# Kernel tuning notes

Measured on AMD Instinct MI355X. Metric: run time of the kernel, lower is better.

The kernel has to match this reference:

```python
import jax, jax.numpy as jnp
import numpy as np

H, D = 16, 64  # num_attention_heads, attention_head_size
BASE = 10000.0

def _rope(q, k, seq_len):
    # RotaryPositionalEmbedding: inv_freq over arange(0, D, 2); emb = cat(freqs, freqs)
    inv_freq = 1.0 / (BASE ** (jnp.arange(0, D, 2, dtype=jnp.float32) / D))  # [D/2]=32
    pos = jnp.arange(seq_len, dtype=jnp.float32)
    freqs = jnp.outer(pos, inv_freq)            # [S, 32]; equals cos_emb[..., :d]
    cos, sin = jnp.cos(freqs), jnp.sin(freqs)   # [S, 32]
    d = D // 2                                   # 32: only first half of head dim rotated
    half = d // 2                                # 16: internal rotate-half within rot part
    def rot(x):  # x: [B, H, S, D]
        xr, xp = x[..., :d], x[..., d:]
        swapped = jnp.concatenate([xr[..., half:], xr[..., :half]], axis=-1)
        xr2 = xr * cos - swapped * sin
        return jnp.concatenate([xr2, xp], axis=-1)
    return rot(q), rot(k)

def setup_inputs() -> dict:
    key = jax.random.key(0)
    ks = jax.random.split(key, 9)
    B, S, E = 2, 2048, 1024
    std = 0.02  # initializer_range
    inp = {"hidden_states": jax.random.normal(ks[0], (B, S, E), jnp.float32)}
    for i, n in enumerate(["q", "k", "v", "d"]):
        inp[f"W{n}"] = jax.random.normal(ks[1 + 2 * i], (E, E), jnp.float32) * std
        inp[f"b{n}"] = jnp.zeros((E,), jnp.float32)
    return inp

def reference(hidden_states, Wq, bq, Wk, bk, Wv, bv, Wd, bd):
    B, S, E = hidden_states.shape
    def heads(x):  # [B,S,E] -> [B,H,S,D]
        return x.reshape(B, S, H, D).transpose(0, 2, 1, 3)
    q = heads(hidden_states @ Wq + bq)
    k = heads(hidden_states @ Wk + bk)
    v = heads(hidden_states @ Wv + bv)
    q, k = _rope(q, k, S)
    scores = jnp.einsum("bhqd,bhkd->bhqk", q, k) / jnp.sqrt(jnp.float32(D))
    causal = jnp.tril(jnp.ones((S, S), dtype=bool))
    scores = jnp.where(causal, scores, -jnp.inf)
    probs = jax.nn.softmax(scores, axis=-1)
    ctx = jnp.einsum("bhqk,bhkd->bhqd", probs, v)
    ctx = ctx.transpose(0, 2, 1, 3).reshape(B, S, E)
    return ctx @ Wd + bd
```

## Files before the change

kernel.cpp:

```cpp
#include <hip/hip_runtime.h>
#include <stdint.h>

typedef __bf16 bf8 __attribute__((ext_vector_type(8)));
typedef float f4 __attribute__((ext_vector_type(4)));
typedef unsigned short us8 __attribute__((ext_vector_type(8)));
typedef unsigned short us4 __attribute__((ext_vector_type(4)));

#define MFMA16(a, b, c) __builtin_amdgcn_mfma_f32_16x16x32_bf16(a, b, c, 0, 0, 0)

__device__ __forceinline__ unsigned short f2b(float f) {
  union { float f; unsigned u; } x; x.f = f;
  unsigned u = x.u;
  u += 0x7fffu + ((u >> 16) & 1u);
  return (unsigned short)(u >> 16);
}

__device__ __forceinline__ unsigned pk2(float a, float b) {
  union { float f; unsigned u; } ua, ub; ua.f = a; ub.f = b;
  return __builtin_amdgcn_perm(ub.u + 0x8000u, ua.u + 0x8000u, 0x07060302u);
}

__global__ __launch_bounds__(256) void cvt_bf16_kernel(
    const float* __restrict__ x, unsigned short* __restrict__ y) {
  int i = blockIdx.x * 256 + threadIdx.x;
  float4 v = ((const float4*)x)[i];
  us4 r = { f2b(v.x), f2b(v.y), f2b(v.z), f2b(v.w) };
  *(us4*)(y + (size_t)i * 4) = r;
}

__global__ __launch_bounds__(256) void transpose_cvt_kernel(
    const float* __restrict__ W, unsigned short* __restrict__ Wt) {
  __shared__ float tile[32][33];
  int tx = threadIdx.x & 31, ty = threadIdx.x >> 5;
  int kb = blockIdx.x * 32, nb = blockIdx.y * 32;
#pragma unroll
  for (int j = 0; j < 32; j += 8)
    tile[ty + j][tx] = W[(size_t)(kb + ty + j) * 1024 + nb + tx];
  __syncthreads();
#pragma unroll
  for (int j = 0; j < 32; j += 8)
    Wt[(size_t)(nb + ty + j) * 1024 + kb + tx] = f2b(tile[tx][ty + j]);
}

#define LDSK 40

__global__ __launch_bounds__(256) void gemm_qkv_kernel(
    const unsigned short* __restrict__ X,
    const unsigned short* __restrict__ Wqt, const unsigned short* __restrict__ Wkt,
    const unsigned short* __restrict__ Wvt,
    const float* __restrict__ bq, const float* __restrict__ bk,
    const float* __restrict__ bv,
    unsigned short* __restrict__ Qo, unsigned short* __restrict__ Ko,
    unsigned short* __restrict__ Vo) {
  const unsigned short* Wt; const float* bias; unsigned short* out;
  if (blockIdx.z == 0)      { Wt = Wqt; bias = bq; out = Qo; }
  else if (blockIdx.z == 1) { Wt = Wkt; bias = bk; out = Ko; }
  else                      { Wt = Wvt; bias = bv; out = Vo; }

  __shared__ unsigned short As[128 * LDSK];
  __shared__ unsigned short Bs[128 * LDSK];
  const int t = threadIdx.x;
  const int wave = t >> 6, lane = t & 63, quad = lane >> 4, l16 = lane & 15;
  const int wm = (wave >> 1) * 64, wn = (wave & 1) * 64;
  const int m0 = blockIdx.y * 128, n0 = blockIdx.x * 128;

  f4 acc[4][4];
#pragma unroll
  for (int mi = 0; mi < 4; ++mi)
#pragma unroll
    for (int ni = 0; ni < 4; ++ni) acc[mi][ni] = (f4)0.0f;

  for (int k0 = 0; k0 < 1024; k0 += 32) {
    __syncthreads();
#pragma unroll
    for (int it = 0; it < 2; ++it) {
      int chunk = t + it * 256;
      int row = chunk >> 2, c8 = (chunk & 3) * 8;
      *(us8*)&As[row * LDSK + c8] =
          *(const us8*)&X[(size_t)(m0 + row) * 1024 + k0 + c8];
      *(us8*)&Bs[row * LDSK + c8] =
          *(const us8*)&Wt[(size_t)(n0 + row) * 1024 + k0 + c8];
    }
    __syncthreads();
    bf8 a[4], b[4];
#pragma unroll
    for (int mi = 0; mi < 4; ++mi)
      a[mi] = *(const bf8*)&As[(wm + mi * 16 + l16) * LDSK + quad * 8];
#pragma unroll
    for (int ni = 0; ni < 4; ++ni)
      b[ni] = *(const bf8*)&Bs[(wn + ni * 16 + l16) * LDSK + quad * 8];
#pragma unroll
    for (int mi = 0; mi < 4; ++mi)
#pragma unroll
      for (int ni = 0; ni < 4; ++ni)
        acc[mi][ni] = MFMA16(a[mi], b[ni], acc[mi][ni]);
  }

  float biasv[4];
#pragma unroll
  for (int ni = 0; ni < 4; ++ni) biasv[ni] = bias[n0 + wn + ni * 16 + l16];

  if (blockIdx.z < 2) {
    const float kr = 13.287712379549449f / 32.0f;
    const float f0 = exp2f(-(float)l16 * kr);
    const float f1 = exp2f(-(float)(l16 + 16) * kr);
    const float qs = (blockIdx.z == 0) ? 0.18033688011112042f : 1.0f;
#pragma unroll
    for (int mi = 0; mi < 4; ++mi) {
#pragma unroll
      for (int r = 0; r < 4; ++r) {
        int m = m0 + wm + mi * 16 + quad * 4 + r;
        float s = (float)(m & 2047);
        float s0, c0, s1, c1;
        __sincosf(s * f0, &s0, &c0);
        __sincosf(s * f1, &s1, &c1);
        float v0 = acc[mi][0][r] + biasv[0];
        float v1 = acc[mi][1][r] + biasv[1];
        acc[mi][0][r] = (v0 * c0 - v1 * s0) * qs;
        acc[mi][1][r] = (v1 * c1 - v0 * s1) * qs;
        acc[mi][2][r] = (acc[mi][2][r] + biasv[2]) * qs;
        acc[mi][3][r] = (acc[mi][3][r] + biasv[3]) * qs;
      }
    }
#pragma unroll
    for (int ni = 0; ni < 4; ++ni) {
      int n = n0 + wn + ni * 16 + l16;
      int h = n >> 6, d = n & 63;
#pragma unroll
      for (int mi = 0; mi < 4; ++mi) {
#pragma unroll
        for (int r = 0; r < 4; ++r) {
          int m = m0 + wm + mi * 16 + quad * 4 + r;
          int b_ = m >> 11, s = m & 2047;
          out[(size_t)(((b_ << 4) | h) * 2048 + s) * 64 + d] = f2b(acc[mi][ni][r]);
        }
      }
    }
  } else {
#pragma unroll
    for (int ni = 0; ni < 4; ++ni) {
      int n = n0 + wn + ni * 16 + l16;
      int h = n >> 6, d = n & 63;
#pragma unroll
      for (int mi = 0; mi < 4; ++mi) {
        int m = m0 + wm + mi * 16 + quad * 4;
        int b_ = m >> 11, s = m & 2047;
        us4 w = { f2b(acc[mi][ni][0] + biasv[ni]), f2b(acc[mi][ni][1] + biasv[ni]),
                  f2b(acc[mi][ni][2] + biasv[ni]), f2b(acc[mi][ni][3] + biasv[ni]) };
        *(us4*)&out[((size_t)(((b_ << 4) | h) * 64 + d)) * 2048 + s] = w;
      }
    }
  }
}

__global__ __launch_bounds__(256) void flash_attn_kernel(
    const unsigned short* __restrict__ Q, const unsigned short* __restrict__ K,
    const unsigned short* __restrict__ Vt, unsigned short* __restrict__ ctx) {
  __shared__ unsigned short PsT[4][16 * 72];

  const int t = threadIdx.x;
  const int wave = t >> 6, lane = t & 63, quad = lane >> 4, l16 = lane & 15;

  const int id = blockIdx.x;
  const int bh = id & 31;
  const int j = id >> 5;
  const int qt = (j >> 3) ? (15 - (j & 7)) : (j & 7);
  const int qbase = qt * 128;
  const int b = bh >> 4, h = bh & 15;

  const unsigned short* Qh = Q + (size_t)bh * 2048 * 64;
  const unsigned short* Kh = K + (size_t)bh * 2048 * 64;
  const unsigned short* Vh = Vt + (size_t)bh * 64 * 2048;

  const int wrow0 = qbase + wave * 32;

  bf8 qb[2][2];
#pragma unroll
  for (int f = 0; f < 2; ++f)
#pragma unroll
    for (int c = 0; c < 2; ++c)
      qb[f][c] = *(const bf8*)&Qh[(size_t)(wrow0 + f * 16 + l16) * 64 + c * 32 + quad * 8];

  us8 ones_u = { 0x3F80, 0x3F80, 0x3F80, 0x3F80, 0x3F80, 0x3F80, 0x3F80, 0x3F80 };
  bf8 ones = *(bf8*)&ones_u;

  f4 o[2][4];
  float mrow[2] = { -3e38f, -3e38f }, lrow[2] = { 0.0f, 0.0f };
#pragma unroll
  for (int f = 0; f < 2; ++f)
#pragma unroll
    for (int dt = 0; dt < 4; ++dt) o[f][dt] = (f4)0.0f;

  unsigned short* myP = &PsT[wave][0];
  const int nkw = (wrow0 >> 6) + 1;

  for (int kt = 0; kt < nkw; ++kt) {
    const int k0 = kt * 64;
    bf8 ka[4][2], va[4][2];
#pragma unroll
    for (int mt = 0; mt < 4; ++mt)
#pragma unroll
      for (int c = 0; c < 2; ++c)
        ka[mt][c] = *(const bf8*)&Kh[(size_t)(k0 + mt * 16 + l16) * 64 + c * 32 + quad * 8];
#pragma unroll
    for (int dt = 0; dt < 4; ++dt)
#pragma unroll
      for (int c = 0; c < 2; ++c)
        va[dt][c] = *(const bf8*)&Vh[(size_t)(dt * 16 + l16) * 2048 + k0 + c * 32 + quad * 8];

#pragma unroll
    for (int f = 0; f < 2; ++f) {
      const int q = wrow0 + f * 16 + l16;
      f4 sc[4];
#pragma unroll
      for (int mt = 0; mt < 4; ++mt) {
        f4 z = (f4)0.0f;
        z = MFMA16(ka[mt][0], qb[f][0], z);
        z = MFMA16(ka[mt][1], qb[f][1], z);
        sc[mt] = z;
      }
      if (k0 + 63 > wrow0 + f * 16) {
#pragma unroll
        for (int mt = 0; mt < 4; ++mt)
#pragma unroll
          for (int r = 0; r < 4; ++r) {
            int kk = k0 + mt * 16 + quad * 4 + r;
            if (kk > q) sc[mt][r] = -3e38f;
          }
      }
      float mx = fmaxf(fmaxf(sc[0][0], sc[0][1]), fmaxf(sc[0][2], sc[0][3]));
#pragma unroll
      for (int mt = 1; mt < 4; ++mt)
        mx = fmaxf(mx, fmaxf(fmaxf(sc[mt][0], sc[mt][1]), fmaxf(sc[mt][2], sc[mt][3])));
      mx = fmaxf(mx, __shfl_xor(mx, 16));
      mx = fmaxf(mx, __shfl_xor(mx, 32));
      float mn = fmaxf(mrow[f], mx);
      float al = exp2f(mrow[f] - mn);
      mrow[f] = mn;
#pragma unroll
      for (int mt = 0; mt < 4; ++mt) {
        float p0 = exp2f(sc[mt][0] - mn), p1 = exp2f(sc[mt][1] - mn);
        float p2 = exp2f(sc[mt][2] - mn), p3 = exp2f(sc[mt][3] - mn);
        uint2 w = { pk2(p0, p1), pk2(p2, p3) };
        *(uint2*)&myP[l16 * 72 + mt * 16 + quad * 4] = w;
      }
#pragma unroll
      for (int dt = 0; dt < 4; ++dt) o[f][dt] *= al;
      __threadfence_block();
      bf8 pb0 = *(const bf8*)&myP[l16 * 72 + quad * 8];
      bf8 pb1 = *(const bf8*)&myP[l16 * 72 + 32 + quad * 8];
      f4 z2 = (f4)0.0f;
      z2 = MFMA16(ones, pb0, z2);
      z2 = MFMA16(ones, pb1, z2);
      lrow[f] = lrow[f] * al + z2[0];
#pragma unroll
      for (int dt = 0; dt < 4; ++dt) {
        o[f][dt] = MFMA16(va[dt][0], pb0, o[f][dt]);
        o[f][dt] = MFMA16(va[dt][1], pb1, o[f][dt]);
      }
    }
  }

#pragma unroll
  for (int f = 0; f < 2; ++f) {
    float inv = 1.0f / lrow[f];
    int q = wrow0 + f * 16 + l16;
#pragma unroll
    for (int dt = 0; dt < 4; ++dt) {
      us4 w = { f2b(o[f][dt][0] * inv), f2b(o[f][dt][1] * inv),
                f2b(o[f][dt][2] * inv), f2b(o[f][dt][3] * inv) };
      *(us4*)&ctx[((size_t)(b * 2048 + q)) * 1024 + h * 64 + dt * 16 + quad * 4] = w;
    }
  }
}

__global__ __launch_bounds__(256) void gemm_out_kernel(
    const unsigned short* __restrict__ A,
    const unsigned short* __restrict__ Wt,
    const float* __restrict__ bias, float* __restrict__ out) {
  __shared__ unsigned short As[128 * LDSK];
  __shared__ unsigned short Bs[128 * LDSK];
  const int t = threadIdx.x;
  const int wave = t >> 6, lane = t & 63, quad = lane >> 4, l16 = lane & 15;
  const int wm = (wave >> 1) * 64, wn = (wave & 1) * 64;
  const int m0 = blockIdx.y * 128, n0 = blockIdx.x * 128;

  f4 acc[4][4];
#pragma unroll
  for (int mi = 0; mi < 4; ++mi)
#pragma unroll
    for (int ni = 0; ni < 4; ++ni) acc[mi][ni] = (f4)0.0f;

  for (int k0 = 0; k0 < 1024; k0 += 32) {
    __syncthreads();
#pragma unroll
    for (int it = 0; it < 2; ++it) {
      int chunk = t + it * 256;
      int row = chunk >> 2, c8 = (chunk & 3) * 8;
      *(us8*)&As[row * LDSK + c8] =
          *(const us8*)&A[(size_t)(m0 + row) * 1024 + k0 + c8];
      *(us8*)&Bs[row * LDSK + c8] =
          *(const us8*)&Wt[(size_t)(n0 + row) * 1024 + k0 + c8];
    }
    __syncthreads();
    bf8 a[4], b[4];
#pragma unroll
    for (int mi = 0; mi < 4; ++mi)
      a[mi] = *(const bf8*)&As[(wm + mi * 16 + l16) * LDSK + quad * 8];
#pragma unroll
    for (int ni = 0; ni < 4; ++ni)
      b[ni] = *(const bf8*)&Bs[(wn + ni * 16 + l16) * LDSK + quad * 8];
#pragma unroll
    for (int mi = 0; mi < 4; ++mi)
#pragma unroll
      for (int ni = 0; ni < 4; ++ni)
        acc[mi][ni] = MFMA16(a[mi], b[ni], acc[mi][ni]);
  }
#pragma unroll
  for (int ni = 0; ni < 4; ++ni) {
    int n = n0 + wn + ni * 16 + l16;
    float bv_ = bias[n];
#pragma unroll
    for (int mi = 0; mi < 4; ++mi) {
#pragma unroll
      for (int r = 0; r < 4; ++r) {
        int m = m0 + wm + mi * 16 + quad * 4 + r;
        out[(size_t)m * 1024 + n] = acc[mi][ni][r] + bv_;
      }
    }
  }
}

extern "C" void kernel_launch(void* const* d_in, const int* in_sizes, int n_in,
                              void* d_out, int out_size, void* d_ws, size_t ws_size,
                              hipStream_t stream) {
  const float* hidden = (const float*)d_in[0];
  const float* Wq = (const float*)d_in[1];
  const float* bq = (const float*)d_in[2];
  const float* Wk = (const float*)d_in[3];
  const float* bk = (const float*)d_in[4];
  const float* Wv = (const float*)d_in[5];
  const float* bv = (const float*)d_in[6];
  const float* Wd = (const float*)d_in[7];
  const float* bd = (const float*)d_in[8];
  float* out = (float*)d_out;

  char* ws = (char*)d_ws;
  unsigned short* Xb  = (unsigned short*)(ws);
  unsigned short* Wqt = (unsigned short*)(ws + ( 8ull << 20));
  unsigned short* Wkt = (unsigned short*)(ws + (10ull << 20));
  unsigned short* Wvt = (unsigned short*)(ws + (12ull << 20));
  unsigned short* Wdt = (unsigned short*)(ws + (14ull << 20));
  unsigned short* Qb  = (unsigned short*)(ws + (16ull << 20));
  unsigned short* Kb  = (unsigned short*)(ws + (24ull << 20));
  unsigned short* Vb  = (unsigned short*)(ws + (32ull << 20));
  unsigned short* Cb  = (unsigned short*)(ws + (40ull << 20));

  cvt_bf16_kernel<<<4096, 256, 0, stream>>>(hidden, Xb);
  dim3 tg(32, 32);
  transpose_cvt_kernel<<<tg, 256, 0, stream>>>(Wq, Wqt);
  transpose_cvt_kernel<<<tg, 256, 0, stream>>>(Wk, Wkt);
  transpose_cvt_kernel<<<tg, 256, 0, stream>>>(Wv, Wvt);
  transpose_cvt_kernel<<<tg, 256, 0, stream>>>(Wd, Wdt);
  gemm_qkv_kernel<<<dim3(8, 32, 3), 256, 0, stream>>>(
      Xb, Wqt, Wkt, Wvt, bq, bk, bv, Qb, Kb, Vb);
  flash_attn_kernel<<<512, 256, 0, stream>>>(Qb, Kb, Vb, Cb);
  gemm_out_kernel<<<dim3(8, 32), 256, 0, stream>>>(Cb, Wdt, bd, out);
}
```

Baseline: 240.9 us.

## Switch flash attention to 32x32 MFMA with K/V double-buffering and merge weight transposes

Rewrites the attention inner loop to use 32x32x16 bf16 MFMA tiles, so each wave handles 32 query rows as one fragment. K/V loads for the next 64-key tile are prefetched into a second register set while the current tile computes. The row sum is now accumulated in VALU with a cross-half shuffle instead of an extra MFMA against a ones vector, and the LDS fence becomes an explicit lgkmcnt wait. The four weight transpose launches are merged into one launch with a z-dimension. Double-buffered fragments raise register pressure, which the occupancy hint of 2 blocks per CU may constrain.

```diff
diff --git a/kernel.cpp b/kernel.cpp
--- a/kernel.cpp
+++ b/kernel.cpp
@@ -3,10 +3,12 @@
 
 typedef __bf16 bf8 __attribute__((ext_vector_type(8)));
 typedef float f4 __attribute__((ext_vector_type(4)));
+typedef float f16v __attribute__((ext_vector_type(16)));
 typedef unsigned short us8 __attribute__((ext_vector_type(8)));
 typedef unsigned short us4 __attribute__((ext_vector_type(4)));
 
 #define MFMA16(a, b, c) __builtin_amdgcn_mfma_f32_16x16x32_bf16(a, b, c, 0, 0, 0)
+#define MFMA32(a, b, c) __builtin_amdgcn_mfma_f32_32x32x16_bf16(a, b, c, 0, 0, 0)
 
 __device__ __forceinline__ unsigned short f2b(float f) {
   union { float f; unsigned u; } x; x.f = f;
@@ -28,8 +30,16 @@
   *(us4*)(y + (size_t)i * 4) = r;
 }
 
-__global__ __launch_bounds__(256) void transpose_cvt_kernel(
-    const float* __restrict__ W, unsigned short* __restrict__ Wt) {
+__global__ __launch_bounds__(256) void transpose_cvt4_kernel(
+    const float* __restrict__ W0, const float* __restrict__ W1,
+    const float* __restrict__ W2, const float* __restrict__ W3,
+    unsigned short* __restrict__ T0, unsigned short* __restrict__ T1,
+    unsigned short* __restrict__ T2, unsigned short* __restrict__ T3) {
+  const float* W; unsigned short* Wt;
+  if (blockIdx.z == 0)      { W = W0; Wt = T0; }
+  else if (blockIdx.z == 1) { W = W1; Wt = T1; }
+  else if (blockIdx.z == 2) { W = W2; Wt = T2; }
+  else                      { W = W3; Wt = T3; }
   __shared__ float tile[32][33];
   int tx = threadIdx.x & 31, ty = threadIdx.x >> 5;
   int kb = blockIdx.x * 32, nb = blockIdx.y * 32;
@@ -153,13 +163,16 @@
   }
 }
 
-__global__ __launch_bounds__(256) void flash_attn_kernel(
+#define PST 72
+
+__global__ __launch_bounds__(256, 2) void flash_attn_kernel(
     const unsigned short* __restrict__ Q, const unsigned short* __restrict__ K,
     const unsigned short* __restrict__ Vt, unsigned short* __restrict__ ctx) {
-  __shared__ unsigned short PsT[4][16 * 72];
+  __shared__ unsigned short PsT[4][32 * PST];
 
   const int t = threadIdx.x;
-  const int wave = t >> 6, lane = t & 63, quad = lane >> 4, l16 = lane & 15;
+  const int wave = t >> 6, lane = t & 63;
+  const int l32 = lane & 31, hl = lane >> 5;
 
   const int id = blockIdx.x;
   const int bh = id & 31;
@@ -173,104 +186,111 @@
   const unsigned short* Vh = Vt + (size_t)bh * 64 * 2048;
 
   const int wrow0 = qbase + wave * 32;
-
-  bf8 qb[2][2];
-#pragma unroll
-  for (int f = 0; f < 2; ++f)
-#pragma unroll
-    for (int c = 0; c < 2; ++c)
-      qb[f][c] = *(const bf8*)&Qh[(size_t)(wrow0 + f * 16 + l16) * 64 + c * 32 + quad * 8];
-
-  us8 ones_u = { 0x3F80, 0x3F80, 0x3F80, 0x3F80, 0x3F80, 0x3F80, 0x3F80, 0x3F80 };
-  bf8 ones = *(bf8*)&ones_u;
-
-  f4 o[2][4];
-  float mrow[2] = { -3e38f, -3e38f }, lrow[2] = { 0.0f, 0.0f };
-#pragma unroll
-  for (int f = 0; f < 2; ++f)
-#pragma unroll
-    for (int dt = 0; dt < 4; ++dt) o[f][dt] = (f4)0.0f;
+  const int q = wrow0 + l32;
+
+  bf8 qb[4];
+#pragma unroll
+  for (int c = 0; c < 4; ++c)
+    qb[c] = *(const bf8*)&Qh[(size_t)q * 64 + c * 16 + hl * 8];
+
+  f16v o0 = (f16v)0.0f, o1 = (f16v)0.0f;
+  float mrow = -3e38f, lrow = 0.0f;
 
   unsigned short* myP = &PsT[wave][0];
   const int nkw = (wrow0 >> 6) + 1;
 
-  for (int kt = 0; kt < nkw; ++kt) {
-    const int k0 = kt * 64;
-    bf8 ka[4][2], va[4][2];
-#pragma unroll
-    for (int mt = 0; mt < 4; ++mt)
-#pragma unroll
-      for (int c = 0; c < 2; ++c)
-        ka[mt][c] = *(const bf8*)&Kh[(size_t)(k0 + mt * 16 + l16) * 64 + c * 32 + quad * 8];
-#pragma unroll
-    for (int dt = 0; dt < 4; ++dt)
-#pragma unroll
-      for (int c = 0; c < 2; ++c)
-        va[dt][c] = *(const bf8*)&Vh[(size_t)(dt * 16 + l16) * 2048 + k0 + c * 32 + quad * 8];
-
-#pragma unroll
-    for (int f = 0; f < 2; ++f) {
-      const int q = wrow0 + f * 16 + l16;
-      f4 sc[4];
-#pragma unroll
-      for (int mt = 0; mt < 4; ++mt) {
-        f4 z = (f4)0.0f;
-        z = MFMA16(ka[mt][0], qb[f][0], z);
-        z = MFMA16(ka[mt][1], qb[f][1], z);
-        sc[mt] = z;
-      }
-      if (k0 + 63 > wrow0 + f * 16) {
-#pragma unroll
-        for (int mt = 0; mt < 4; ++mt)
-#pragma unroll
-          for (int r = 0; r < 4; ++r) {
-            int kk = k0 + mt * 16 + quad * 4 + r;
-            if (kk > q) sc[mt][r] = -3e38f;
-          }
-      }
-      float mx = fmaxf(fmaxf(sc[0][0], sc[0][1]), fmaxf(sc[0][2], sc[0][3]));
-#pragma unroll
-      for (int mt = 1; mt < 4; ++mt)
-        mx = fmaxf(mx, fmaxf(fmaxf(sc[mt][0], sc[mt][1]), fmaxf(sc[mt][2], sc[mt][3])));
-      mx = fmaxf(mx, __shfl_xor(mx, 16));
-      mx = fmaxf(mx, __shfl_xor(mx, 32));
-      float mn = fmaxf(mrow[f], mx);
-      float al = exp2f(mrow[f] - mn);
-      mrow[f] = mn;
-#pragma unroll
-      for (int mt = 0; mt < 4; ++mt) {
-        float p0 = exp2f(sc[mt][0] - mn), p1 = exp2f(sc[mt][1] - mn);
-        float p2 = exp2f(sc[mt][2] - mn), p3 = exp2f(sc[mt][3] - mn);
-        uint2 w = { pk2(p0, p1), pk2(p2, p3) };
-        *(uint2*)&myP[l16 * 72 + mt * 16 + quad * 4] = w;
-      }
-#pragma unroll
-      for (int dt = 0; dt < 4; ++dt) o[f][dt] *= al;
-      __threadfence_block();
-      bf8 pb0 = *(const bf8*)&myP[l16 * 72 + quad * 8];
-      bf8 pb1 = *(const bf8*)&myP[l16 * 72 + 32 + quad * 8];
-      f4 z2 = (f4)0.0f;
-      z2 = MFMA16(ones, pb0, z2);
-      z2 = MFMA16(ones, pb1, z2);
-      lrow[f] = lrow[f] * al + z2[0];
-#pragma unroll
-      for (int dt = 0; dt < 4; ++dt) {
-        o[f][dt] = MFMA16(va[dt][0], pb0, o[f][dt]);
-        o[f][dt] = MFMA16(va[dt][1], pb1, o[f][dt]);
-      }
-    }
-  }
-
-#pragma unroll
-  for (int f = 0; f < 2; ++f) {
-    float inv = 1.0f / lrow[f];
-    int q = wrow0 + f * 16 + l16;
-#pragma unroll
-    for (int dt = 0; dt < 4; ++dt) {
-      us4 w = { f2b(o[f][dt][0] * inv), f2b(o[f][dt][1] * inv),
-                f2b(o[f][dt][2] * inv), f2b(o[f][dt][3] * inv) };
-      *(us4*)&ctx[((size_t)(b * 2048 + q)) * 1024 + h * 64 + dt * 16 + quad * 4] = w;
-    }
+  bf8 kfA[2][4], vfA[2][4], kfB[2][4], vfB[2][4];
+
+  auto loadK = [&](bf8 (&kf)[2][4], int k0) {
+#pragma unroll
+    for (int mt = 0; mt < 2; ++mt)
+#pragma unroll
+      for (int c = 0; c < 4; ++c)
+        kf[mt][c] = *(const bf8*)&Kh[(size_t)(k0 + mt * 32 + l32) * 64 + c * 16 + hl * 8];
+  };
+  auto loadV = [&](bf8 (&vf)[2][4], int k0) {
+#pragma unroll
+    for (int dt = 0; dt < 2; ++dt)
+#pragma unroll
+      for (int c = 0; c < 4; ++c)
+        vf[dt][c] = *(const bf8*)&Vh[(size_t)(dt * 32 + l32) * 2048 + k0 + c * 16 + hl * 8];
+  };
+
+  auto step = [&](int k0, bf8 (&kf)[2][4], bf8 (&vf)[2][4]) {
+    f16v s0 = (f16v)0.0f, s1 = (f16v)0.0f;
+#pragma unroll
+    for (int c = 0; c < 4; ++c) {
+      s0 = MFMA32(kf[0][c], qb[c], s0);
+      s1 = MFMA32(kf[1][c], qb[c], s1);
+    }
+    if (k0 + 64 > wrow0) {
+#pragma unroll
+      for (int g = 0; g < 4; ++g)
+#pragma unroll
+        for (int i = 0; i < 4; ++i) {
+          int kk = k0 + g * 8 + hl * 4 + i;
+          if (kk > q) s0[g * 4 + i] = -3e38f;
+          if (kk + 32 > q) s1[g * 4 + i] = -3e38f;
+        }
+    }
+    float mx = fmaxf(s0[0], s1[0]);
+#pragma unroll
+    for (int i = 1; i < 16; ++i) mx = fmaxf(mx, fmaxf(s0[i], s1[i]));
+    mx = fmaxf(mx, __shfl_xor(mx, 32));
+    float mn = fmaxf(mrow, mx);
+    float al = exp2f(mrow - mn);
+    mrow = mn;
+    float sum = 0.0f;
+#pragma unroll
+    for (int g = 0; g < 4; ++g) {
+      float p0 = exp2f(s0[g * 4 + 0] - mn), p1 = exp2f(s0[g * 4 + 1] - mn);
+      float p2 = exp2f(s0[g * 4 + 2] - mn), p3 = exp2f(s0[g * 4 + 3] - mn);
+      sum += (p0 + p1) + (p2 + p3);
+      uint2 w = { pk2(p0, p1), pk2(p2, p3) };
+      *(uint2*)&myP[l32 * PST + g * 8 + hl * 4] = w;
+      float r0 = exp2f(s1[g * 4 + 0] - mn), r1 = exp2f(s1[g * 4 + 1] - mn);
+      float r2 = exp2f(s1[g * 4 + 2] - mn), r3 = exp2f(s1[g * 4 + 3] - mn);
+      sum += (r0 + r1) + (r2 + r3);
+      uint2 w2 = { pk2(r0, r1), pk2(r2, r3) };
+      *(uint2*)&myP[l32 * PST + 32 + g * 8 + hl * 4] = w2;
+    }
+#pragma unroll
+    for (int i = 0; i < 16; ++i) { o0[i] *= al; o1[i] *= al; }
+    asm volatile("s_waitcnt lgkmcnt(0)" ::: "memory");
+    bf8 pb[4];
+#pragma unroll
+    for (int c = 0; c < 4; ++c)
+      pb[c] = *(const bf8*)&myP[l32 * PST + c * 16 + hl * 8];
+#pragma unroll
+    for (int c = 0; c < 4; ++c) {
+      o0 = MFMA32(vf[0][c], pb[c], o0);
+      o1 = MFMA32(vf[1][c], pb[c], o1);
+    }
+    sum += __shfl_xor(sum, 32);
+    lrow = lrow * al + sum;
+  };
+
+  loadK(kfA, 0); loadV(vfA, 0);
+  int kt = 0;
+  while (true) {
+    if (kt + 1 < nkw) { loadK(kfB, (kt + 1) * 64); loadV(vfB, (kt + 1) * 64); }
+    step(kt * 64, kfA, vfA);
+    ++kt; if (kt >= nkw) break;
+    if (kt + 1 < nkw) { loadK(kfA, (kt + 1) * 64); loadV(vfA, (kt + 1) * 64); }
+    step(kt * 64, kfB, vfB);
+    ++kt; if (kt >= nkw) break;
+  }
+
+  float inv = 1.0f / lrow;
+#pragma unroll
+  for (int g = 0; g < 4; ++g) {
+    int d0 = g * 8 + hl * 4;
+    us4 w0 = { f2b(o0[g * 4 + 0] * inv), f2b(o0[g * 4 + 1] * inv),
+               f2b(o0[g * 4 + 2] * inv), f2b(o0[g * 4 + 3] * inv) };
+    *(us4*)&ctx[((size_t)(b * 2048 + q)) * 1024 + h * 64 + d0] = w0;
+    us4 w1 = { f2b(o1[g * 4 + 0] * inv), f2b(o1[g * 4 + 1] * inv),
+               f2b(o1[g * 4 + 2] * inv), f2b(o1[g * 4 + 3] * inv) };
+    *(us4*)&ctx[((size_t)(b * 2048 + q)) * 1024 + h * 64 + 32 + d0] = w1;
   }
 }
 
@@ -357,11 +377,8 @@
   unsigned short* Cb  = (unsigned short*)(ws + (40ull << 20));
 
   cvt_bf16_kernel<<<4096, 256, 0, stream>>>(hidden, Xb);
-  dim3 tg(32, 32);
-  transpose_cvt_kernel<<<tg, 256, 0, stream>>>(Wq, Wqt);
-  transpose_cvt_kernel<<<tg, 256, 0, stream>>>(Wk, Wkt);
-  transpose_cvt_kernel<<<tg, 256, 0, stream>>>(Wv, Wvt);
-  transpose_cvt_kernel<<<tg, 256, 0, stream>>>(Wd, Wdt);
+  transpose_cvt4_kernel<<<dim3(32, 32, 4), 256, 0, stream>>>(
+      Wq, Wk, Wv, Wd, Wqt, Wkt, Wvt, Wdt);
   gemm_qkv_kernel<<<dim3(8, 32, 3), 256, 0, stream>>>(
       Xb, Wqt, Wkt, Wvt, bq, bk, bv, Qb, Kb, Vb);
   flash_attn_kernel<<<512, 256, 0, stream>>>(Qb, Kb, Vb, Cb);
```

Result: faster. 236.1 us (-2.0%).
